# Performance work log

Measured on AMD Instinct MI355X. Metric: run time of the kernel, lower is better.

## Reference

```python
import jax, jax.numpy as jnp
import numpy as np
from jax import lax

B, C_IN, N, C_OUT, K = 16, 128, 2048, 256, 20
EPS = 1e-5


def setup_inputs() -> dict:
    key = jax.random.key(0)
    k1, k2 = jax.random.split(key)
    x = jax.random.normal(k1, (B, C_IN, N), dtype=jnp.float32)
    W = jax.random.normal(k2, (C_OUT, 2 * C_IN), dtype=jnp.float32) * (1.0 / np.sqrt(2 * C_IN))
    gamma = jnp.ones((C_OUT,), dtype=jnp.float32)
    beta = jnp.zeros((C_OUT,), dtype=jnp.float32)
    return {"x": x, "W": W, "gamma": gamma, "beta": beta, "k": K}


def _knn_inds(x, k):
    # squared pairwise distance: (B, N, N); computed with no grad (stop_gradient)
    xs = lax.stop_gradient(x)
    inner = jnp.einsum('bcn,bcm->bnm', xs, xs)
    sq = jnp.sum(xs * xs, axis=1)  # (B, N)
    pd = sq[:, :, None] - 2.0 * inner + sq[:, None, :]
    _, inds = lax.top_k(-pd, k)  # smallest distances -> (B, N, k)
    return inds


def reference(x, W, gamma, beta, k):
    knn = _knn_inds(x, k)                                   # (B, N, k) int
    # gather neighbours: neigh[b,c,n,j] = x[b,c,knn[b,n,j]]
    neigh = jax.vmap(lambda xb, kb: xb[:, kb])(x, knn)      # (B, C, N, k)
    central = jnp.broadcast_to(x[:, :, :, None], neigh.shape)
    edge = jnp.concatenate([central, neigh - central], axis=1)  # (B, 2C, N, k)
    # 1x1 conv (bias-free) as GEMM
    y = jnp.einsum('oc,bcnk->bonk', W, edge)                # (B, C_out, N, k)
    # BatchNorm2d (training-mode batch stats) + affine
    mean = jnp.mean(y, axis=(0, 2, 3), keepdims=True)
    var = jnp.var(y, axis=(0, 2, 3), keepdims=True)
    y = (y - mean) * lax.rsqrt(var + EPS)
    y = y * gamma[None, :, None, None] + beta[None, :, None, None]
    y = jax.nn.relu(y)
    return jnp.max(y, axis=3)                               # (B, C_out, N)
```

## Files before the change

kernel.cpp:

```cpp
#include <hip/hip_runtime.h>

#define B_   16
#define CIN  128
#define NPT  2048
#define COUT 256
#define KNN  20
#define KEEP 16
#define CAND 64
#define SIFT 32
#define EPS  1e-5f
#define DBIAS 256.0f

#define SQ_OFF   0ull
#define IDX_OFF  131072ull
#define UT_OFF   2752512ull
#define VT_OFF   36306944ull
#define GS_OFF   69861376ull
#define ST_OFF   69865472ull
#define AMAX_OFF 69871616ull
#define AMIN_OFF 103426048ull
#define WS_NEED_FUSED 136980480ull
#define XT_OFF   UT_OFF
#define XHT_OFF  VT_OFF

typedef _Float16 f16x8 __attribute__((ext_vector_type(8)));
typedef float    f32x4 __attribute__((ext_vector_type(4)));
typedef float    f32x2 __attribute__((ext_vector_type(2)));

__global__ __launch_bounds__(256) void prep_kernel(const float* __restrict__ x,
                                                   float* __restrict__ xT,
                                                   _Float16* __restrict__ xhT,
                                                   float* __restrict__ sqh) {
    __shared__ float Ls[128 * 68];
    __shared__ float ps[4 * 64];
    const int b = blockIdx.y, n0 = blockIdx.x * 64, t = threadIdx.x;
    const float* xb = x + (size_t)b * CIN * NPT;
    #pragma unroll
    for (int e = 0; e < 8; ++e) {
        int f = e * 256 + t;
        int c = f >> 4, n4 = (f & 15) << 2;
        *(float4*)&Ls[c * 68 + n4] = *(const float4*)&xb[(size_t)c * NPT + n0 + n4];
    }
    __syncthreads();
    {
        int nl = t & 63, part = t >> 6;
        float acc = 0.f;
        #pragma unroll
        for (int j = 0; j < 32; ++j) {
            float vh = (float)(_Float16)Ls[(part * 32 + j) * 68 + nl];
            acc += vh * vh;
        }
        ps[part * 64 + nl] = acc;
    }
    #pragma unroll
    for (int e = 0; e < 2; ++e) {
        int u = e * 256 + t;
        int nl = u >> 3, ck = (u & 7) << 4;
        float vv[16];
        #pragma unroll
        for (int j = 0; j < 16; ++j) vv[j] = Ls[(ck + j) * 68 + nl];
        size_t row = (size_t)b * NPT + n0 + nl;
        #pragma unroll
        for (int j = 0; j < 4; ++j) {
            float4 w = {vv[4 * j], vv[4 * j + 1], vv[4 * j + 2], vv[4 * j + 3]};
            *(float4*)&xT[row * CIN + ck + 4 * j] = w;
        }
        f16x8 h0, h1;
        #pragma unroll
        for (int j = 0; j < 8; ++j) { h0[j] = (_Float16)vv[j]; h1[j] = (_Float16)vv[8 + j]; }
        *(f16x8*)&xhT[row * CIN + ck] = h0;
        *(f16x8*)&xhT[row * CIN + ck + 8] = h1;
    }
    __syncthreads();
    if (t < 64) sqh[b * NPT + n0 + t] = ps[t] + ps[64 + t] + ps[128 + t] + ps[192 + t];
}

__global__ void wconv_kernel(const float* __restrict__ W,
                             _Float16* __restrict__ Wu,
                             _Float16* __restrict__ Wv) {
    int gid = blockIdx.x * 256 + threadIdx.x;
    int o = gid >> 7, c = gid & 127;
    float w1 = W[o * 256 + c], w2 = W[o * 256 + 128 + c];
    Wu[gid] = (_Float16)(w1 - w2);
    Wv[gid] = (_Float16)w2;
}

__device__ __forceinline__ void stage_pts(const _Float16* __restrict__ xhb,
                                          _Float16* buf, int base_n, int t) {
    const int l15 = t & 15, ks = t >> 6;
    const int quad = (t >> 4) & 3;
    const int c = ks * 32 + quad * 8;
    #pragma unroll
    for (int e = 0; e < 4; ++e) {
        const int n = base_n + e * 16 + l15;
        const _Float16* src = xhb + (size_t)n * CIN + c;
        _Float16* dst = buf + (size_t)(e * 256 + (t & 192)) * 8;
        __builtin_amdgcn_global_load_lds(
            (const __attribute__((address_space(1))) void*)src,
            (__attribute__((address_space(3))) void*)dst, 16, 0, 0);
    }
}

__device__ __forceinline__ void stage_tile16(const _Float16* __restrict__ srcl,
                                             _Float16* dsthalf) {
    #pragma unroll
    for (int e = 0; e < 4; ++e) {
        __builtin_amdgcn_global_load_lds(
            (const __attribute__((address_space(1))) void*)(srcl + e * 32),
            (__attribute__((address_space(3))) void*)(dsthalf + (size_t)e * 512),
            16, 0, 0);
    }
}

__global__ __launch_bounds__(256, 2) void knn_kernel(const _Float16* __restrict__ xhT,
                                                     const float* __restrict__ sqh,
                                                     int* __restrict__ surv_out) {
    __shared__ char smraw[59392];
    _Float16* bufA = (_Float16*)smraw;
    float*    sqm  = (float*)(smraw + 18432);

    const int id  = blockIdx.x;
    const int xcd = id & 7, qq = id >> 3;
    const int b   = xcd + ((qq >> 5) << 3);
    const int q0  = (qq & 31) * 64;
    const int t  = threadIdx.x;
    const int lane = t & 63, wv = t >> 6;
    const int l15 = lane & 15, quad = lane >> 4;
    const _Float16* xhb = xhT + (size_t)b * NPT * CIN;

    #pragma unroll
    for (int e = 0; e < 8; ++e)
        sqm[e * 256 + t] = sqh[b * NPT + e * 256 + t] + DBIAS;

    stage_pts(xhb, bufA, q0, t);
    __syncthreads();

    f16x8 af[4][4];
    #pragma unroll
    for (int qh = 0; qh < 4; ++qh)
        #pragma unroll
        for (int ks = 0; ks < 4; ++ks)
            af[qh][ks] = *(const f16x8*)(bufA + (size_t)((qh * 4 + ks) * 64 + lane) * 8);
    __syncthreads();

    _Float16* wbuf = (_Float16*)(smraw + 26624 + wv * 8192);
    float*    DtW  = (float*)(smraw + wv * 4608);
    const _Float16* srcl = xhb + (size_t)(wv * 16 + l15) * CIN + quad * 8;

    stage_tile16(srcl, wbuf);

    float bd[KEEP];
    #pragma unroll
    for (int i = 0; i < KEEP; ++i) bd[i] = 3.0e38f;

    #pragma unroll 1
    for (int ss = 0; ss < 32; ++ss) {
        const int mb = ss * 64 + wv * 16;
        asm volatile("s_waitcnt vmcnt(0)" ::: "memory");
        __builtin_amdgcn_sched_barrier(0);
        const _Float16* cur = wbuf + (ss & 1) * 2048;
        f16x8 bf[4];
        #pragma unroll
        for (int ks = 0; ks < 4; ++ks)
            bf[ks] = *(const f16x8*)(cur + ks * 512 + lane * 8);
        float sm_ = sqm[mb + l15];
        asm volatile("s_waitcnt lgkmcnt(0)" ::: "memory");
        __builtin_amdgcn_sched_barrier(0);
        if (ss < 31)
            stage_tile16(srcl + (size_t)(ss + 1) * 64 * CIN,
                         wbuf + ((ss + 1) & 1) * 2048);
        __builtin_amdgcn_sched_barrier(0);
        f32x4 acc[4];
        #pragma unroll
        for (int qh = 0; qh < 4; ++qh) acc[qh] = (f32x4){0.f, 0.f, 0.f, 0.f};
        #pragma unroll
        for (int ks = 0; ks < 4; ++ks)
            #pragma unroll
            for (int qh = 0; qh < 4; ++qh)
                acc[qh] = __builtin_amdgcn_mfma_f32_16x16x32_f16(af[qh][ks], bf[ks], acc[qh], 0, 0, 0);
        const unsigned om = (unsigned)(mb + l15);
        #pragma unroll
        for (int qh = 0; qh < 4; ++qh) {
            #pragma unroll
            for (int rg = 0; rg < 4; ++rg) {
                int q = qh * 16 + quad * 4 + rg;
                float d = sm_ - 2.f * acc[qh][rg];
                DtW[q * 18 + l15] = __uint_as_float((__float_as_uint(d) & 0xFFFFF800u) | om);
            }
        }
        float nk[16];
        {
            const float* myrow = DtW + lane * 18;
            #pragma unroll
            for (int p = 0; p < 8; ++p) {
                f32x2 v = *(const f32x2*)(myrow + 2 * p);
                nk[2 * p] = v[0]; nk[2 * p + 1] = v[1];
            }
        }
        #pragma unroll
        for (int kk = 2; kk <= 16; kk <<= 1) {
            #pragma unroll
            for (int j = kk >> 1; j > 0; j >>= 1) {
                #pragma unroll
                for (int i = 0; i < 16; ++i) {
                    int p = i ^ j;
                    if (p > i) {
                        float a = nk[i], c = nk[p];
                        float lo = fminf(a, c), hi = fmaxf(a, c);
                        if ((i & kk) == 0) { nk[i] = lo; nk[p] = hi; }
                        else               { nk[i] = hi; nk[p] = lo; }
                    }
                }
            }
        }
        #pragma unroll
        for (int i = 0; i < 16; ++i) bd[i] = fminf(bd[i], nk[15 - i]);
        #pragma unroll
        for (int j = 8; j > 0; j >>= 1) {
            #pragma unroll
            for (int i = 0; i < 16; ++i) {
                int p = i ^ j;
                if (p > i) {
                    float a = bd[i], c = bd[p];
                    bd[i] = fminf(a, c);
                    bd[p] = fmaxf(a, c);
                }
            }
        }
    }

    __syncthreads();

    float* Keys = (float*)smraw;
    #pragma unroll
    for (int i = 0; i < KEEP; ++i)
        Keys[lane * 65 + wv * KEEP + i] = bd[i];
    __syncthreads();
    {
        int cnt[KEEP];
        #pragma unroll
        for (int i = 0; i < KEEP; ++i) cnt[i] = 0;
        #pragma unroll 4
        for (int j = 0; j < CAND; ++j) {
            float kj = Keys[lane * 65 + j];
            #pragma unroll
            for (int i = 0; i < KEEP; ++i)
                cnt[i] += (kj < bd[i]) ? 1 : 0;
        }
        int* dst = surv_out + ((size_t)b * NPT + q0 + lane) * SIFT;
        #pragma unroll
        for (int i = 0; i < KEEP; ++i)
            if (cnt[i] < SIFT)
                dst[cnt[i]] = (int)(__float_as_uint(bd[i]) & 0x7FFu);
    }
}

__global__ __launch_bounds__(256, 4) void refine_kernel(const float* __restrict__ xT,
                                                        const int* __restrict__ surv,
                                                        int* __restrict__ knn_out) {
    __shared__ float  Qs[16 * 128];
    __shared__ int    sidx[16 * 32];
    __shared__ double ddL[16 * 32];
    const int id  = blockIdx.x;
    const int xcd = id & 7, qq = id >> 3;
    const int b   = xcd + ((qq >> 7) << 3);
    const int q0  = (qq & 127) * 16;
    const int t = threadIdx.x;
    const float* xTb = xT + (size_t)b * NPT * CIN;
    #pragma unroll
    for (int e = 0; e < 2; ++e)
        sidx[e * 256 + t] = surv[((size_t)b * NPT + q0) * SIFT + e * 256 + t];
    #pragma unroll
    for (int e = 0; e < 2; ++e) {
        int f = e * 256 + t;
        int row = f >> 5, c4 = (f & 31) << 2;
        *(float4*)&Qs[row * 128 + c4] = *(const float4*)&xTb[(size_t)(q0 + row) * CIN + c4];
    }
    __syncthreads();
    const int g = t >> 3, j = t & 7;
    #pragma unroll 1
    for (int it = 0; it < 16; ++it) {
        int pair = it * 32 + g;
        int q = pair >> 5, k = pair & 31;
        int m = sidx[q * 32 + k];
        const float* mrow = xTb + (size_t)m * CIN + j * 16;
        const float* qrow = Qs + q * 128 + j * 16;
        float4 a0 = *(const float4*)&mrow[0];
        float4 a1 = *(const float4*)&mrow[4];
        float4 a2 = *(const float4*)&mrow[8];
        float4 a3 = *(const float4*)&mrow[12];
        float4 c0 = *(const float4*)&qrow[0];
        float4 c1 = *(const float4*)&qrow[4];
        float4 c2 = *(const float4*)&qrow[8];
        float4 c3 = *(const float4*)&qrow[12];
        double ss = 0.0, d0;
        d0 = (double)c0.x - (double)a0.x; ss = fma(d0, d0, ss);
        d0 = (double)c0.y - (double)a0.y; ss = fma(d0, d0, ss);
        d0 = (double)c0.z - (double)a0.z; ss = fma(d0, d0, ss);
        d0 = (double)c0.w - (double)a0.w; ss = fma(d0, d0, ss);
        d0 = (double)c1.x - (double)a1.x; ss = fma(d0, d0, ss);
        d0 = (double)c1.y - (double)a1.y; ss = fma(d0, d0, ss);
        d0 = (double)c1.z - (double)a1.z; ss = fma(d0, d0, ss);
        d0 = (double)c1.w - (double)a1.w; ss = fma(d0, d0, ss);
        d0 = (double)c2.x - (double)a2.x; ss = fma(d0, d0, ss);
        d0 = (double)c2.y - (double)a2.y; ss = fma(d0, d0, ss);
        d0 = (double)c2.z - (double)a2.z; ss = fma(d0, d0, ss);
        d0 = (double)c2.w - (double)a2.w; ss = fma(d0, d0, ss);
        d0 = (double)c3.x - (double)a3.x; ss = fma(d0, d0, ss);
        d0 = (double)c3.y - (double)a3.y; ss = fma(d0, d0, ss);
        d0 = (double)c3.z - (double)a3.z; ss = fma(d0, d0, ss);
        d0 = (double)c3.w - (double)a3.w; ss = fma(d0, d0, ss);
        ss += __shfl_xor(ss, 1, 8);
        ss += __shfl_xor(ss, 2, 8);
        ss += __shfl_xor(ss, 4, 8);
        if (j == 0) ddL[q * 32 + k] = ss;
    }
    __syncthreads();
    const int q = t >> 4, kk = (t & 15) << 1;
    int* dst = knn_out + ((size_t)b * NPT + q0 + q) * KNN;
    #pragma unroll
    for (int e = 0; e < 2; ++e) {
        int k = kk + e;
        double mine = ddL[q * 32 + k];
        int c = 0;
        #pragma unroll 4
        for (int jx = 0; jx < SIFT; ++jx)
            c += (ddL[q * 32 + jx] < mine) ? 1 : 0;
        if (c < KNN) dst[c] = sidx[q * 32 + k];
    }
}

__global__ __launch_bounds__(256, 2) void knn_kernel_fb(const _Float16* __restrict__ xhT,
                                                        const float* __restrict__ xT,
                                                        const float* __restrict__ sqh,
                                                        int* __restrict__ knn_out) {
    __shared__ char smraw[59392];
    _Float16* bufA = (_Float16*)smraw;
    float*    sqm  = (float*)(smraw + 18432);

    const int b  = blockIdx.y;
    const int q0 = blockIdx.x * 64;
    const int t  = threadIdx.x;
    const int lane = t & 63, wv = t >> 6;
    const int l15 = lane & 15, quad = lane >> 4;
    const _Float16* xhb = xhT + (size_t)b * NPT * CIN;

    #pragma unroll
    for (int e = 0; e < 8; ++e)
        sqm[e * 256 + t] = sqh[b * NPT + e * 256 + t] + DBIAS;

    stage_pts(xhb, bufA, q0, t);
    __syncthreads();

    f16x8 af[4][4];
    #pragma unroll
    for (int qh = 0; qh < 4; ++qh)
        #pragma unroll
        for (int ks = 0; ks < 4; ++ks)
            af[qh][ks] = *(const f16x8*)(bufA + (size_t)((qh * 4 + ks) * 64 + lane) * 8);
    __syncthreads();

    _Float16* wbuf = (_Float16*)(smraw + 26624 + wv * 8192);
    float*    DtW  = (float*)(smraw + wv * 4608);
    const _Float16* srcl = xhb + (size_t)(wv * 16 + l15) * CIN + quad * 8;
    stage_tile16(srcl, wbuf);

    float bd[KEEP];
    #pragma unroll
    for (int i = 0; i < KEEP; ++i) bd[i] = 3.0e38f;

    #pragma unroll 1
    for (int ss = 0; ss < 32; ++ss) {
        const int mb = ss * 64 + wv * 16;
        asm volatile("s_waitcnt vmcnt(0)" ::: "memory");
        __builtin_amdgcn_sched_barrier(0);
        const _Float16* cur = wbuf + (ss & 1) * 2048;
        f16x8 bf[4];
        #pragma unroll
        for (int ks = 0; ks < 4; ++ks)
            bf[ks] = *(const f16x8*)(cur + ks * 512 + lane * 8);
        float sm_ = sqm[mb + l15];
        asm volatile("s_waitcnt lgkmcnt(0)" ::: "memory");
        __builtin_amdgcn_sched_barrier(0);
        if (ss < 31)
            stage_tile16(srcl + (size_t)(ss + 1) * 64 * CIN,
                         wbuf + ((ss + 1) & 1) * 2048);
        __builtin_amdgcn_sched_barrier(0);
        f32x4 acc[4];
        #pragma unroll
        for (int qh = 0; qh < 4; ++qh) acc[qh] = (f32x4){0.f, 0.f, 0.f, 0.f};
        #pragma unroll
        for (int ks = 0; ks < 4; ++ks)
            #pragma unroll
            for (int qh = 0; qh < 4; ++qh)
                acc[qh] = __builtin_amdgcn_mfma_f32_16x16x32_f16(af[qh][ks], bf[ks], acc[qh], 0, 0, 0);
        const unsigned om = (unsigned)(mb + l15);
        #pragma unroll
        for (int qh = 0; qh < 4; ++qh) {
            #pragma unroll
            for (int rg = 0; rg < 4; ++rg) {
                int q = qh * 16 + quad * 4 + rg;
                float d = sm_ - 2.f * acc[qh][rg];
                DtW[q * 18 + l15] = __uint_as_float((__float_as_uint(d) & 0xFFFFF800u) | om);
            }
        }
        float nk[16];
        {
            const float* myrow = DtW + lane * 18;
            #pragma unroll
            for (int p = 0; p < 8; ++p) {
                f32x2 v = *(const f32x2*)(myrow + 2 * p);
                nk[2 * p] = v[0]; nk[2 * p + 1] = v[1];
            }
        }
        #pragma unroll
        for (int kk = 2; kk <= 16; kk <<= 1) {
            #pragma unroll
            for (int j = kk >> 1; j > 0; j >>= 1) {
                #pragma unroll
                for (int i = 0; i < 16; ++i) {
                    int p = i ^ j;
                    if (p > i) {
                        float a = nk[i], c = nk[p];
                        float lo = fminf(a, c), hi = fmaxf(a, c);
                        if ((i & kk) == 0) { nk[i] = lo; nk[p] = hi; }
                        else               { nk[i] = hi; nk[p] = lo; }
                    }
                }
            }
        }
        #pragma unroll
        for (int i = 0; i < 16; ++i) bd[i] = fminf(bd[i], nk[15 - i]);
        #pragma unroll
        for (int j = 8; j > 0; j >>= 1) {
            #pragma unroll
            for (int i = 0; i < 16; ++i) {
                int p = i ^ j;
                if (p > i) {
                    float a = bd[i], c = bd[p];
                    bd[i] = fminf(a, c);
                    bd[p] = fmaxf(a, c);
                }
            }
        }
    }

    __syncthreads();

    float*  Keys = (float*)smraw;
    int*    Surv = (int*)(smraw + 16640);
    double* ddL  = (double*)(smraw + 25088);
    #pragma unroll
    for (int i = 0; i < KEEP; ++i)
        Keys[lane * 65 + wv * KEEP + i] = bd[i];
    __syncthreads();
    {
        int cnt[KEEP];
        #pragma unroll
        for (int i = 0; i < KEEP; ++i) cnt[i] = 0;
        #pragma unroll 4
        for (int j = 0; j < CAND; ++j) {
            float kj = Keys[lane * 65 + j];
            #pragma unroll
            for (int i = 0; i < KEEP; ++i)
                cnt[i] += (kj < bd[i]) ? 1 : 0;
        }
        __syncthreads();
        #pragma unroll
        for (int i = 0; i < KEEP; ++i)
            if (cnt[i] < SIFT)
                Surv[lane * 33 + cnt[i]] = (int)(__float_as_uint(bd[i]) & 0x7FFu);
    }
    __syncthreads();

    int ms[8];
    #pragma unroll
    for (int k = 0; k < 8; ++k) ms[k] = Surv[lane * 33 + wv * 8 + k] & 2047;
    double dd8[8];
    #pragma unroll
    for (int k = 0; k < 8; ++k) dd8[k] = 0.0;
    const float* xTb = xT + (size_t)b * NPT * CIN;
    const float* qrow = xTb + (size_t)(q0 + lane) * CIN;
    #pragma unroll 1
    for (int ch = 0; ch < 8; ++ch) {
        double qd[16];
        #pragma unroll
        for (int j = 0; j < 4; ++j) {
            float4 qv = *(const float4*)&qrow[ch * 16 + 4 * j];
            qd[4 * j] = (double)qv.x; qd[4 * j + 1] = (double)qv.y;
            qd[4 * j + 2] = (double)qv.z; qd[4 * j + 3] = (double)qv.w;
        }
        #pragma unroll
        for (int k = 0; k < 8; ++k) {
            const float* mrow = xTb + (size_t)ms[k] * CIN + ch * 16;
            float4 ma = *(const float4*)&mrow[0];
            float4 mb2 = *(const float4*)&mrow[4];
            float4 mc = *(const float4*)&mrow[8];
            float4 md = *(const float4*)&mrow[12];
            double ss = dd8[k], d0;
            d0 = qd[0]  - (double)ma.x;  ss = fma(d0, d0, ss);
            d0 = qd[1]  - (double)ma.y;  ss = fma(d0, d0, ss);
            d0 = qd[2]  - (double)ma.z;  ss = fma(d0, d0, ss);
            d0 = qd[3]  - (double)ma.w;  ss = fma(d0, d0, ss);
            d0 = qd[4]  - (double)mb2.x; ss = fma(d0, d0, ss);
            d0 = qd[5]  - (double)mb2.y; ss = fma(d0, d0, ss);
            d0 = qd[6]  - (double)mb2.z; ss = fma(d0, d0, ss);
            d0 = qd[7]  - (double)mb2.w; ss = fma(d0, d0, ss);
            d0 = qd[8]  - (double)mc.x;  ss = fma(d0, d0, ss);
            d0 = qd[9]  - (double)mc.y;  ss = fma(d0, d0, ss);
            d0 = qd[10] - (double)mc.z;  ss = fma(d0, d0, ss);
            d0 = qd[11] - (double)mc.w;  ss = fma(d0, d0, ss);
            d0 = qd[12] - (double)md.x;  ss = fma(d0, d0, ss);
            d0 = qd[13] - (double)md.y;  ss = fma(d0, d0, ss);
            d0 = qd[14] - (double)md.z;  ss = fma(d0, d0, ss);
            d0 = qd[15] - (double)md.w;  ss = fma(d0, d0, ss);
            dd8[k] = ss;
        }
    }
    #pragma unroll
    for (int k = 0; k < 8; ++k) ddL[lane * 33 + wv * 8 + k] = dd8[k];
    __syncthreads();
    int* dst = knn_out + ((size_t)b * NPT + q0 + lane) * KNN;
    #pragma unroll
    for (int k = 0; k < 8; ++k) {
        int c = 0;
        #pragma unroll 4
        for (int j = 0; j < SIFT; ++j)
            c += (ddL[lane * 33 + j] < dd8[k]) ? 1 : 0;
        if (c < KNN) dst[c] = ms[k];
    }
}

__global__ __launch_bounds__(256) void uv_gemm_h(const _Float16* __restrict__ xhT,
                                                 const _Float16* __restrict__ Wu,
                                                 const _Float16* __restrict__ Wv,
                                                 float* __restrict__ uT,
                                                 float* __restrict__ vT) {
    __shared__ _Float16 Bx[8192];
    const int b = blockIdx.y, n0 = blockIdx.x * 64, t = threadIdx.x;
    const int lane = t & 63, w = t >> 6, l15 = lane & 15, quad = lane >> 4;
    stage_pts(xhT + (size_t)b * NPT * CIN, Bx, n0, t);
    __syncthreads();
    f16x8 bf[4];
    #pragma unroll
    for (int ks = 0; ks < 4; ++ks)
        bf[ks] = *(const f16x8*)(Bx + (size_t)((w * 4 + ks) * 64 + lane) * 8);
    const int n = n0 + w * 16 + l15;
    #pragma unroll 1
    for (int ot = 0; ot < 16; ++ot) {
        const _Float16* wu = Wu + (size_t)(ot * 16 + l15) * 128 + quad * 8;
        const _Float16* wv2 = Wv + (size_t)(ot * 16 + l15) * 128 + quad * 8;
        f32x4 au = (f32x4){0.f, 0.f, 0.f, 0.f};
        f32x4 av = (f32x4){0.f, 0.f, 0.f, 0.f};
        #pragma unroll
        for (int ks = 0; ks < 4; ++ks) {
            f16x8 a_u = *(const f16x8*)(wu + ks * 32);
            f16x8 a_v = *(const f16x8*)(wv2 + ks * 32);
            au = __builtin_amdgcn_mfma_f32_16x16x32_f16(a_u, bf[ks], au, 0, 0, 0);
            av = __builtin_amdgcn_mfma_f32_16x16x32_f16(a_v, bf[ks], av, 0, 0, 0);
        }
        size_t base = ((size_t)b * NPT + n) * COUT + ot * 16 + quad * 4;
        *(f32x4*)&uT[base] = au;
        *(f32x4*)&vT[base] = av;
    }
}

__global__ __launch_bounds__(256) void uv_gemm(const float* __restrict__ x,
                                               const float* __restrict__ W,
                                               float* __restrict__ uT,
                                               float* __restrict__ vT) {
    __shared__ float Ax[32 * 64];
    __shared__ float Bu[32 * 68];
    __shared__ float Bv[32 * 68];
    const int b  = blockIdx.z;
    const int n0 = blockIdx.x * 64;
    const int o0 = blockIdx.y * 64;
    const int t  = threadIdx.x;
    const int tx = t & 15, ty = t >> 4;
    const float* xb = x + (size_t)b * CIN * NPT;
    float au[4][4], av_[4][4];
    #pragma unroll
    for (int i = 0; i < 4; ++i)
        #pragma unroll
        for (int j = 0; j < 4; ++j) { au[i][j] = 0.f; av_[i][j] = 0.f; }
    #pragma unroll 1
    for (int kc = 0; kc < 4; ++kc) {
        const int c0 = kc * 32;
        __syncthreads();
        #pragma unroll
        for (int e = 0; e < 2; ++e) {
            int f = e * 256 + t;
            int cz = f >> 4, ni = (f & 15) << 2;
            *(float4*)&Ax[(cz << 6) + ni] = *(const float4*)&xb[(size_t)(c0 + cz) * NPT + n0 + ni];
        }
        #pragma unroll
        for (int e = 0; e < 8; ++e) {
            int ii = e * 256 + t;
            int cz = ii & 31, oj = ii >> 5;
            float w1 = W[(size_t)(o0 + oj) * 256 + c0 + cz];
            float w2 = W[(size_t)(o0 + oj) * 256 + 128 + c0 + cz];
            Bu[cz * 68 + oj] = w1 - w2;
            Bv[cz * 68 + oj] = w2;
        }
        __syncthreads();
        #pragma unroll 8
        for (int cz = 0; cz < 32; ++cz) {
            const float4 a4 = *(const float4*)&Ax[(cz << 6) + (tx << 2)];
            float bu0 = Bu[cz * 68 + (ty << 2) + 0], bv0 = Bv[cz * 68 + (ty << 2) + 0];
            float bu1 = Bu[cz * 68 + (ty << 2) + 1], bv1 = Bv[cz * 68 + (ty << 2) + 1];
            float bu2 = Bu[cz * 68 + (ty << 2) + 2], bv2 = Bv[cz * 68 + (ty << 2) + 2];
            float bu3 = Bu[cz * 68 + (ty << 2) + 3], bv3 = Bv[cz * 68 + (ty << 2) + 3];
            au[0][0] += a4.x * bu0; au[0][1] += a4.x * bu1; au[0][2] += a4.x * bu2; au[0][3] += a4.x * bu3;
            au[1][0] += a4.y * bu0; au[1][1] += a4.y * bu1; au[1][2] += a4.y * bu2; au[1][3] += a4.y * bu3;
            au[2][0] += a4.z * bu0; au[2][1] += a4.z * bu1; au[2][2] += a4.z * bu2; au[2][3] += a4.z * bu3;
            au[3][0] += a4.w * bu0; au[3][1] += a4.w * bu1; au[3][2] += a4.w * bu2; au[3][3] += a4.w * bu3;
            av_[0][0] += a4.x * bv0; av_[0][1] += a4.x * bv1; av_[0][2] += a4.x * bv2; av_[0][3] += a4.x * bv3;
            av_[1][0] += a4.y * bv0; av_[1][1] += a4.y * bv1; av_[1][2] += a4.y * bv2; av_[1][3] += a4.y * bv3;
            av_[2][0] += a4.z * bv0; av_[2][1] += a4.z * bv1; av_[2][2] += a4.z * bv2; av_[2][3] += a4.z * bv3;
            av_[3][0] += a4.w * bv0; av_[3][1] += a4.w * bv1; av_[3][2] += a4.w * bv2; av_[3][3] += a4.w * bv3;
        }
    }
    #pragma unroll
    for (int i = 0; i < 4; ++i) {
        int n = n0 + (tx << 2) + i;
        size_t base = ((size_t)b * NPT + n) * COUT + o0 + (ty << 2);
        float4 u4 = {au[i][0], au[i][1], au[i][2], au[i][3]};
        float4 v4 = {av_[i][0], av_[i][1], av_[i][2], av_[i][3]};
        *(float4*)&uT[base] = u4;
        *(float4*)&vT[base] = v4;
    }
}

__global__ __launch_bounds__(256) void gather_stats(const float* __restrict__ uT,
                                                    const float* __restrict__ vT,
                                                    const int* __restrict__ knn_in,
                                                    double* __restrict__ gsum,
                                                    float* __restrict__ aMax,
                                                    float* __restrict__ aMin) {
    __shared__ int sidx[16 * KNN];
    const int id  = blockIdx.x;
    const int xcd = id & 7, qq = id >> 3;
    const int b   = xcd + ((qq >> 7) << 3);
    const int inner = qq & 127;
    const int n0  = (inner >> 2) * 64 + (inner & 3) * 16;
    const int o   = threadIdx.x;
    for (int e = o; e < 16 * KNN; e += 256)
        sidx[e] = knn_in[((size_t)b * NPT + n0) * KNN + e];
    __syncthreads();
    const float* ub = uT + ((size_t)b * NPT + n0) * COUT + o;
    const float* vb = vT + (size_t)b * NPT * COUT + o;
    float* amx = aMax + ((size_t)b * NPT + n0) * COUT + o;
    float* amn = aMin + ((size_t)b * NPT + n0) * COUT + o;
    double s1 = 0.0, s2 = 0.0;
    #pragma unroll 1
    for (int s = 0; s < 16; ++s) {
        float u = ub[(size_t)s * COUT];
        float vmax = -3e38f, vmin = 3e38f, vsum = 0.f, vsq = 0.f;
        #pragma unroll
        for (int j = 0; j < KNN; ++j) {
            float v = vb[(size_t)sidx[s * KNN + j] * COUT];
            vmax = fmaxf(vmax, v);
            vmin = fminf(vmin, v);
            vsum += v;
            vsq = fmaf(v, v, vsq);
        }
        s1 += 20.0 * (double)u + (double)vsum;
        s2 += 20.0 * (double)u * (double)u + 2.0 * (double)u * (double)vsum + (double)vsq;
        float y1 = u + vmax;
        float y2 = u + vmin;
        __builtin_nontemporal_store(y1, &amx[(size_t)s * COUT]);
        __builtin_nontemporal_store(y2, &amn[(size_t)s * COUT]);
    }
    atomicAdd(&gsum[o], s1);
    atomicAdd(&gsum[COUT + o], s2);
}

__global__ __launch_bounds__(256) void stats_kernel(const float* __restrict__ uT,
                                                    const float* __restrict__ vT,
                                                    const int* __restrict__ knn_in,
                                                    double* __restrict__ gsum) {
    __shared__ int sidx[64 * KNN];
    const int b  = blockIdx.y;
    const int n0 = blockIdx.x * 64;
    const int o  = threadIdx.x;
    for (int e = o; e < 64 * KNN; e += 256)
        sidx[e] = knn_in[((size_t)b * NPT + n0) * KNN + e];
    __syncthreads();
    const float* ub = uT + ((size_t)b * NPT + n0) * COUT + o;
    const float* vb = vT + (size_t)b * NPT * COUT + o;
    double s1 = 0.0, s2 = 0.0;
    #pragma unroll 1
    for (int s = 0; s < 64; ++s) {
        float u = ub[(size_t)s * COUT];
        #pragma unroll
        for (int j = 0; j < KNN; ++j) {
            float y = u + vb[(size_t)sidx[s * KNN + j] * COUT];
            s1 += (double)y;
            s2 = fma((double)y, (double)y, s2);
        }
    }
    atomicAdd(&gsum[o], s1);
    atomicAdd(&gsum[COUT + o], s2);
}

__global__ void finalize_kernel(const double* __restrict__ gsum,
                                const float* __restrict__ gamma,
                                const float* __restrict__ beta,
                                float* __restrict__ st) {
    const int o = threadIdx.x;
    const double M = (double)B_ * NPT * KNN;
    double mean = gsum[o] / M;
    double var  = gsum[COUT + o] / M - mean * mean;
    float inv = 1.0f / sqrtf((float)var + EPS);
    float s = gamma[o] * inv;
    st[o] = s;
    st[COUT + o] = beta[o] - (float)mean * s;
}

__global__ __launch_bounds__(256, 2) void out2_kernel(const float* __restrict__ aMax,
                                                      const float* __restrict__ aMin,
                                                      const float* __restrict__ st,
                                                      float* __restrict__ out) {
    __shared__ float zt[256 * 68];
    const int b  = blockIdx.y;
    const int n0 = blockIdx.x * 64;
    const int o  = threadIdx.x;
    const float s  = st[o];
    const float tt = st[COUT + o];
    const float* amx = aMax + ((size_t)b * NPT + n0) * COUT + o;
    const float* amn = aMin + ((size_t)b * NPT + n0) * COUT + o;
    #pragma unroll 2
    for (int si = 0; si < 64; ++si) {
        float y1 = amx[(size_t)si * COUT];
        float y2 = amn[(size_t)si * COUT];
        float z1 = fmaxf(s * y1 + tt, 0.f);
        float z2 = fmaxf(s * y2 + tt, 0.f);
        zt[o * 68 + si] = fmaxf(z1, z2);
    }
    __syncthreads();
    float* dst = out + ((size_t)b * COUT + o) * NPT + n0;
    #pragma unroll
    for (int i = 0; i < 16; ++i)
        *(float4*)&dst[i * 4] = *(const float4*)&zt[o * 68 + i * 4];
}

__global__ __launch_bounds__(256, 2) void out_kernel(const float* __restrict__ uT,
                                                     const float* __restrict__ vT,
                                                     const int* __restrict__ knn_in,
                                                     const float* __restrict__ st,
                                                     float* __restrict__ out) {
    __shared__ int sidx[64 * KNN];
    __shared__ float zt[256 * 68];
    const int b  = blockIdx.y;
    const int n0 = blockIdx.x * 64;
    const int o  = threadIdx.x;
    for (int e = o; e < 64 * KNN; e += 256)
        sidx[e] = knn_in[((size_t)b * NPT + n0) * KNN + e];
    __syncthreads();
    const float s  = st[o];
    const float tt = st[COUT + o];
    const float* ub = uT + ((size_t)b * NPT + n0) * COUT + o;
    const float* vb = vT + (size_t)b * NPT * COUT + o;
    #pragma unroll 1
    for (int si = 0; si < 64; ++si) {
        float u = ub[(size_t)si * COUT];
        float ymax = -3e38f, ymin = 3e38f;
        #pragma unroll
        for (int j = 0; j < KNN; ++j) {
            float y = u + vb[(size_t)sidx[si * KNN + j] * COUT];
            ymax = fmaxf(ymax, y);
            ymin = fminf(ymin, y);
        }
        float z1 = fmaxf(s * ymax + tt, 0.f);
        float z2 = fmaxf(s * ymin + tt, 0.f);
        zt[o * 68 + si] = fmaxf(z1, z2);
    }
    __syncthreads();
    float* dst = out + ((size_t)b * COUT + o) * NPT + n0;
    #pragma unroll
    for (int i = 0; i < 16; ++i)
        *(float4*)&dst[i * 4] = *(const float4*)&zt[o * 68 + i * 4];
}

extern "C" void kernel_launch(void* const* d_in, const int* in_sizes, int n_in,
                              void* d_out, int out_size, void* d_ws, size_t ws_size,
                              hipStream_t stream) {
    const float* x     = (const float*)d_in[0];
    const float* W     = (const float*)d_in[1];
    const float* gamma = (const float*)d_in[2];
    const float* beta  = (const float*)d_in[3];
    float* out = (float*)d_out;
    char* ws = (char*)d_ws;
    float*     sqh  = (float*)(ws + SQ_OFF);
    int*       idx  = (int*)(ws + IDX_OFF);
    float*     uT   = (float*)(ws + UT_OFF);
    float*     vT   = (float*)(ws + VT_OFF);
    double*    gsum = (double*)(ws + GS_OFF);
    float*     st   = (float*)(ws + ST_OFF);
    float*     aMax = (float*)(ws + AMAX_OFF);
    float*     aMin = (float*)(ws + AMIN_OFF);
    const bool fused = (ws_size >= WS_NEED_FUSED);

    hipMemsetAsync(gsum, 0, 2 * COUT * sizeof(double), stream);
    if (fused) {
        float*    xT  = (float*)(ws + AMAX_OFF);
        _Float16* xhT = (_Float16*)(ws + AMAX_OFF + 16777216ull);
        _Float16* Wu  = (_Float16*)(ws + AMAX_OFF + 25165824ull);
        _Float16* Wv  = (_Float16*)(ws + AMAX_OFF + 25231360ull);
        int*      svG = (int*)(ws + UT_OFF);
        prep_kernel<<<dim3(32, 16), 256, 0, stream>>>(x, xT, xhT, sqh);
        wconv_kernel<<<128, 256, 0, stream>>>(W, Wu, Wv);
        knn_kernel<<<512, 256, 0, stream>>>(xhT, sqh, svG);
        refine_kernel<<<2048, 256, 0, stream>>>(xT, svG, idx);
        uv_gemm_h<<<dim3(32, 16), 256, 0, stream>>>(xhT, Wu, Wv, uT, vT);
        gather_stats<<<2048, 256, 0, stream>>>(uT, vT, idx, gsum, aMax, aMin);
        finalize_kernel<<<1, 256, 0, stream>>>(gsum, gamma, beta, st);
        out2_kernel<<<dim3(32, 16), 256, 0, stream>>>(aMax, aMin, st, out);
    } else {
        float*    xT  = (float*)(ws + XT_OFF);
        _Float16* xhT = (_Float16*)(ws + XHT_OFF);
        prep_kernel<<<dim3(32, 16), 256, 0, stream>>>(x, xT, xhT, sqh);
        knn_kernel_fb<<<dim3(32, 16), 256, 0, stream>>>(xhT, xT, sqh, idx);
        uv_gemm<<<dim3(32, 4, 16), 256, 0, stream>>>(x, W, uT, vT);
        stats_kernel<<<dim3(32, 16), 256, 0, stream>>>(uT, vT, idx, gsum);
        finalize_kernel<<<1, 256, 0, stream>>>(gsum, gamma, beta, st);
        out_kernel<<<dim3(32, 16), 256, 0, stream>>>(uT, vT, idx, st, out);
    }
}
```

Measured before the change: 307.6 us.

## Halve knn query tile to 32 points, doubling blocks and occupancy

The knn kernel now processes 32 query points per block instead of 64, which doubles the grid to 1024 blocks, shrinks shared memory and raises launch bounds to 4 blocks per CU. Each lane sorts 8 candidates per tile instead of 16, merged into the upper half of its top-16 list. The final sift now compares across 128 keys (8 sub-lists per query) instead of 64. The double-buffered prefetch of the next tile is removed in favour of a synchronous load each iteration, relying on higher occupancy to hide latency; it also re-reads the candidate points twice as often across blocks.

```diff
diff --git a/kernel.cpp b/kernel.cpp
--- a/kernel.cpp
+++ b/kernel.cpp
@@ -6,7 +6,6 @@
 #define COUT 256
 #define KNN  20
 #define KEEP 16
-#define CAND 64
 #define SIFT 32
 #define EPS  1e-5f
 #define DBIAS 256.0f
@@ -101,6 +100,22 @@
     }
 }
 
+__device__ __forceinline__ void stage_pts32(const _Float16* __restrict__ xhb,
+                                            _Float16* buf, int base_n, int t) {
+    const int l15 = t & 15, ks = t >> 6;
+    const int quad = (t >> 4) & 3;
+    const int c = ks * 32 + quad * 8;
+    #pragma unroll
+    for (int e = 0; e < 2; ++e) {
+        const int n = base_n + e * 16 + l15;
+        const _Float16* src = xhb + (size_t)n * CIN + c;
+        _Float16* dst = buf + (size_t)(e * 256 + (t & 192)) * 8;
+        __builtin_amdgcn_global_load_lds(
+            (const __attribute__((address_space(1))) void*)src,
+            (__attribute__((address_space(3))) void*)dst, 16, 0, 0);
+    }
+}
+
 __device__ __forceinline__ void stage_tile16(const _Float16* __restrict__ srcl,
                                              _Float16* dsthalf) {
     #pragma unroll
@@ -112,18 +127,18 @@
     }
 }
 
-__global__ __launch_bounds__(256, 2) void knn_kernel(const _Float16* __restrict__ xhT,
+__global__ __launch_bounds__(256, 4) void knn_kernel(const _Float16* __restrict__ xhT,
                                                      const float* __restrict__ sqh,
                                                      int* __restrict__ surv_out) {
-    __shared__ char smraw[59392];
+    __shared__ char smraw[33792];
     _Float16* bufA = (_Float16*)smraw;
-    float*    sqm  = (float*)(smraw + 18432);
+    float*    sqm  = (float*)(smraw + 25600);
 
     const int id  = blockIdx.x;
     const int xcd = id & 7, qq = id >> 3;
-    const int b   = xcd + ((qq >> 5) << 3);
-    const int q0  = (qq & 31) * 64;
-    const int t  = threadIdx.x;
+    const int b   = xcd + ((qq >> 6) << 3);
+    const int q0  = (qq & 63) * 32;
+    const int t   = threadIdx.x;
     const int lane = t & 63, wv = t >> 6;
     const int l15 = lane & 15, quad = lane >> 4;
     const _Float16* xhb = xhT + (size_t)b * NPT * CIN;
@@ -132,22 +147,20 @@
     for (int e = 0; e < 8; ++e)
         sqm[e * 256 + t] = sqh[b * NPT + e * 256 + t] + DBIAS;
 
-    stage_pts(xhb, bufA, q0, t);
-    __syncthreads();
-
-    f16x8 af[4][4];
-    #pragma unroll
-    for (int qh = 0; qh < 4; ++qh)
-        #pragma unroll
-        for (int ks = 0; ks < 4; ++ks)
-            af[qh][ks] = *(const f16x8*)(bufA + (size_t)((qh * 4 + ks) * 64 + lane) * 8);
-    __syncthreads();
-
-    _Float16* wbuf = (_Float16*)(smraw + 26624 + wv * 8192);
-    float*    DtW  = (float*)(smraw + wv * 4608);
+    stage_pts32(xhb, bufA, q0, t);
+    __syncthreads();
+
+    f16x8 af0[4], af1[4];
+    #pragma unroll
+    for (int ks = 0; ks < 4; ++ks) {
+        af0[ks] = *(const f16x8*)(bufA + (size_t)((ks)*64 + lane) * 8);
+        af1[ks] = *(const f16x8*)(bufA + (size_t)((4 + ks) * 64 + lane) * 8);
+    }
+    __syncthreads();
+
+    _Float16* wbuf = (_Float16*)(smraw + 9216 + wv * 4096);
+    float*    DtW  = (float*)(smraw + wv * 2304);
     const _Float16* srcl = xhb + (size_t)(wv * 16 + l15) * CIN + quad * 8;
-
-    stage_tile16(srcl, wbuf);
 
     float bd[KEEP];
     #pragma unroll
@@ -156,53 +169,49 @@
     #pragma unroll 1
     for (int ss = 0; ss < 32; ++ss) {
         const int mb = ss * 64 + wv * 16;
+        stage_tile16(srcl + (size_t)ss * 64 * CIN, wbuf);
+        float sm_ = sqm[mb + l15];
         asm volatile("s_waitcnt vmcnt(0)" ::: "memory");
         __builtin_amdgcn_sched_barrier(0);
-        const _Float16* cur = wbuf + (ss & 1) * 2048;
-        f16x8 bf[4];
-        #pragma unroll
-        for (int ks = 0; ks < 4; ++ks)
-            bf[ks] = *(const f16x8*)(cur + ks * 512 + lane * 8);
-        float sm_ = sqm[mb + l15];
-        asm volatile("s_waitcnt lgkmcnt(0)" ::: "memory");
-        __builtin_amdgcn_sched_barrier(0);
-        if (ss < 31)
-            stage_tile16(srcl + (size_t)(ss + 1) * 64 * CIN,
-                         wbuf + ((ss + 1) & 1) * 2048);
-        __builtin_amdgcn_sched_barrier(0);
-        f32x4 acc[4];
-        #pragma unroll
-        for (int qh = 0; qh < 4; ++qh) acc[qh] = (f32x4){0.f, 0.f, 0.f, 0.f};
-        #pragma unroll
-        for (int ks = 0; ks < 4; ++ks)
-            #pragma unroll
-            for (int qh = 0; qh < 4; ++qh)
-                acc[qh] = __builtin_amdgcn_mfma_f32_16x16x32_f16(af[qh][ks], bf[ks], acc[qh], 0, 0, 0);
+        f16x8 bf0 = *(const f16x8*)(wbuf + 0 * 512 + lane * 8);
+        f16x8 bf1 = *(const f16x8*)(wbuf + 1 * 512 + lane * 8);
+        f16x8 bf2 = *(const f16x8*)(wbuf + 2 * 512 + lane * 8);
+        f16x8 bf3 = *(const f16x8*)(wbuf + 3 * 512 + lane * 8);
+        f32x4 acc0 = (f32x4){0.f, 0.f, 0.f, 0.f};
+        f32x4 acc1 = (f32x4){0.f, 0.f, 0.f, 0.f};
+        acc0 = __builtin_amdgcn_mfma_f32_16x16x32_f16(af0[0], bf0, acc0, 0, 0, 0);
+        acc1 = __builtin_amdgcn_mfma_f32_16x16x32_f16(af1[0], bf0, acc1, 0, 0, 0);
+        acc0 = __builtin_amdgcn_mfma_f32_16x16x32_f16(af0[1], bf1, acc0, 0, 0, 0);
+        acc1 = __builtin_amdgcn_mfma_f32_16x16x32_f16(af1[1], bf1, acc1, 0, 0, 0);
+        acc0 = __builtin_amdgcn_mfma_f32_16x16x32_f16(af0[2], bf2, acc0, 0, 0, 0);
+        acc1 = __builtin_amdgcn_mfma_f32_16x16x32_f16(af1[2], bf2, acc1, 0, 0, 0);
+        acc0 = __builtin_amdgcn_mfma_f32_16x16x32_f16(af0[3], bf3, acc0, 0, 0, 0);
+        acc1 = __builtin_amdgcn_mfma_f32_16x16x32_f16(af1[3], bf3, acc1, 0, 0, 0);
         const unsigned om = (unsigned)(mb + l15);
         #pragma unroll
-        for (int qh = 0; qh < 4; ++qh) {
-            #pragma unroll
-            for (int rg = 0; rg < 4; ++rg) {
-                int q = qh * 16 + quad * 4 + rg;
-                float d = sm_ - 2.f * acc[qh][rg];
-                DtW[q * 18 + l15] = __uint_as_float((__float_as_uint(d) & 0xFFFFF800u) | om);
-            }
-        }
-        float nk[16];
+        for (int rg = 0; rg < 4; ++rg) {
+            float d0 = sm_ - 2.f * acc0[rg];
+            DtW[(quad * 4 + rg) * 18 + l15] =
+                __uint_as_float((__float_as_uint(d0) & 0xFFFFF800u) | om);
+            float d1 = sm_ - 2.f * acc1[rg];
+            DtW[(16 + quad * 4 + rg) * 18 + l15] =
+                __uint_as_float((__float_as_uint(d1) & 0xFFFFF800u) | om);
+        }
+        float nk[8];
         {
-            const float* myrow = DtW + lane * 18;
-            #pragma unroll
-            for (int p = 0; p < 8; ++p) {
+            const float* myrow = DtW + (lane & 31) * 18 + (lane >> 5) * 8;
+            #pragma unroll
+            for (int p = 0; p < 4; ++p) {
                 f32x2 v = *(const f32x2*)(myrow + 2 * p);
                 nk[2 * p] = v[0]; nk[2 * p + 1] = v[1];
             }
         }
         #pragma unroll
-        for (int kk = 2; kk <= 16; kk <<= 1) {
+        for (int kk = 2; kk <= 8; kk <<= 1) {
             #pragma unroll
             for (int j = kk >> 1; j > 0; j >>= 1) {
                 #pragma unroll
-                for (int i = 0; i < 16; ++i) {
+                for (int i = 0; i < 8; ++i) {
                     int p = i ^ j;
                     if (p > i) {
                         float a = nk[i], c = nk[p];
@@ -214,7 +223,7 @@
             }
         }
         #pragma unroll
-        for (int i = 0; i < 16; ++i) bd[i] = fminf(bd[i], nk[15 - i]);
+        for (int i = 0; i < 8; ++i) bd[8 + i] = fminf(bd[8 + i], nk[7 - i]);
         #pragma unroll
         for (int j = 8; j > 0; j >>= 1) {
             #pragma unroll
@@ -232,22 +241,24 @@
     __syncthreads();
 
     float* Keys = (float*)smraw;
+    const int qy  = lane & 31;
+    const int sub = wv * 2 + (lane >> 5);
     #pragma unroll
     for (int i = 0; i < KEEP; ++i)
-        Keys[lane * 65 + wv * KEEP + i] = bd[i];
+        Keys[qy * 129 + sub * KEEP + i] = bd[i];
     __syncthreads();
     {
         int cnt[KEEP];
         #pragma unroll
         for (int i = 0; i < KEEP; ++i) cnt[i] = 0;
         #pragma unroll 4
-        for (int j = 0; j < CAND; ++j) {
-            float kj = Keys[lane * 65 + j];
+        for (int j = 0; j < 128; ++j) {
+            float kj = Keys[qy * 129 + j];
             #pragma unroll
             for (int i = 0; i < KEEP; ++i)
                 cnt[i] += (kj < bd[i]) ? 1 : 0;
         }
-        int* dst = surv_out + ((size_t)b * NPT + q0 + lane) * SIFT;
+        int* dst = surv_out + ((size_t)b * NPT + q0 + qy) * SIFT;
         #pragma unroll
         for (int i = 0; i < KEEP; ++i)
             if (cnt[i] < SIFT)
@@ -459,7 +470,7 @@
         #pragma unroll
         for (int i = 0; i < KEEP; ++i) cnt[i] = 0;
         #pragma unroll 4
-        for (int j = 0; j < CAND; ++j) {
+        for (int j = 0; j < 64; ++j) {
             float kj = Keys[lane * 65 + j];
             #pragma unroll
             for (int i = 0; i < KEEP; ++i)
@@ -810,7 +821,7 @@
         int*      svG = (int*)(ws + UT_OFF);
         prep_kernel<<<dim3(32, 16), 256, 0, stream>>>(x, xT, xhT, sqh);
         wconv_kernel<<<128, 256, 0, stream>>>(W, Wu, Wv);
-        knn_kernel<<<512, 256, 0, stream>>>(xhT, sqh, svG);
+        knn_kernel<<<1024, 256, 0, stream>>>(xhT, sqh, svG);
         refine_kernel<<<2048, 256, 0, stream>>>(xT, svG, idx);
         uv_gemm_h<<<dim3(32, 16), 256, 0, stream>>>(xhT, Wu, Wv, uT, vT);
         gather_stats<<<2048, 256, 0, stream>>>(uT, vT, idx, gsum, aMax, aMin);
```

Measured after the change: 364.5 us. 1.19x slower.

## Split KNN candidate scan across eight waves per block, drop double buffering

Applied to the files above, without the earlier changes.

The KNN kernel now runs 512 threads per block, so eight waves share the candidate columns and the outer loop takes 16 steps instead of 32. Each wave loads its tile synchronously into a single LDS buffer instead of prefetching the next tile into a double buffer. The final per-query merge therefore ranks 128 kept candidates instead of 64. This trades the load/compute overlap, and possibly registers under the tighter launch bound, for more waves to hide latency. The LDS footprint also grows.

```diff
diff --git a/kernel.cpp b/kernel.cpp
--- a/kernel.cpp
+++ b/kernel.cpp
@@ -6,7 +6,6 @@
 #define COUT 256
 #define KNN  20
 #define KEEP 16
-#define CAND 64
 #define SIFT 32
 #define EPS  1e-5f
 #define DBIAS 256.0f
@@ -112,27 +111,27 @@
     }
 }
 
-__global__ __launch_bounds__(256, 2) void knn_kernel(const _Float16* __restrict__ xhT,
+__global__ __launch_bounds__(512, 4) void knn_kernel(const _Float16* __restrict__ xhT,
                                                      const float* __restrict__ sqh,
                                                      int* __restrict__ surv_out) {
-    __shared__ char smraw[59392];
+    __shared__ char smraw[77824];
     _Float16* bufA = (_Float16*)smraw;
-    float*    sqm  = (float*)(smraw + 18432);
+    float*    sqm  = (float*)(smraw + 69632);
 
     const int id  = blockIdx.x;
     const int xcd = id & 7, qq = id >> 3;
     const int b   = xcd + ((qq >> 5) << 3);
     const int q0  = (qq & 31) * 64;
-    const int t  = threadIdx.x;
+    const int t   = threadIdx.x;
     const int lane = t & 63, wv = t >> 6;
     const int l15 = lane & 15, quad = lane >> 4;
     const _Float16* xhb = xhT + (size_t)b * NPT * CIN;
 
     #pragma unroll
-    for (int e = 0; e < 8; ++e)
-        sqm[e * 256 + t] = sqh[b * NPT + e * 256 + t] + DBIAS;
-
-    stage_pts(xhb, bufA, q0, t);
+    for (int e = 0; e < 4; ++e)
+        sqm[e * 512 + t] = sqh[b * NPT + e * 512 + t] + DBIAS;
+
+    if (wv < 4) stage_pts(xhb, bufA, q0, t);
     __syncthreads();
 
     f16x8 af[4][4];
@@ -143,41 +142,35 @@
             af[qh][ks] = *(const f16x8*)(bufA + (size_t)((qh * 4 + ks) * 64 + lane) * 8);
     __syncthreads();
 
-    _Float16* wbuf = (_Float16*)(smraw + 26624 + wv * 8192);
+    _Float16* wbuf = (_Float16*)(smraw + 36864 + wv * 4096);
     float*    DtW  = (float*)(smraw + wv * 4608);
     const _Float16* srcl = xhb + (size_t)(wv * 16 + l15) * CIN + quad * 8;
 
-    stage_tile16(srcl, wbuf);
-
     float bd[KEEP];
     #pragma unroll
     for (int i = 0; i < KEEP; ++i) bd[i] = 3.0e38f;
 
     #pragma unroll 1
-    for (int ss = 0; ss < 32; ++ss) {
-        const int mb = ss * 64 + wv * 16;
+    for (int ss = 0; ss < 16; ++ss) {
+        const int mb = ss * 128 + wv * 16;
+        stage_tile16(srcl + (size_t)ss * 128 * CIN, wbuf);
+        float sm_ = sqm[mb + l15];
         asm volatile("s_waitcnt vmcnt(0)" ::: "memory");
         __builtin_amdgcn_sched_barrier(0);
-        const _Float16* cur = wbuf + (ss & 1) * 2048;
-        f16x8 bf[4];
-        #pragma unroll
-        for (int ks = 0; ks < 4; ++ks)
-            bf[ks] = *(const f16x8*)(cur + ks * 512 + lane * 8);
-        float sm_ = sqm[mb + l15];
-        asm volatile("s_waitcnt lgkmcnt(0)" ::: "memory");
-        __builtin_amdgcn_sched_barrier(0);
-        if (ss < 31)
-            stage_tile16(srcl + (size_t)(ss + 1) * 64 * CIN,
-                         wbuf + ((ss + 1) & 1) * 2048);
-        __builtin_amdgcn_sched_barrier(0);
+        f16x8 bf0 = *(const f16x8*)(wbuf + 0 * 512 + lane * 8);
+        f16x8 bf1 = *(const f16x8*)(wbuf + 1 * 512 + lane * 8);
+        f16x8 bf2 = *(const f16x8*)(wbuf + 2 * 512 + lane * 8);
+        f16x8 bf3 = *(const f16x8*)(wbuf + 3 * 512 + lane * 8);
         f32x4 acc[4];
         #pragma unroll
         for (int qh = 0; qh < 4; ++qh) acc[qh] = (f32x4){0.f, 0.f, 0.f, 0.f};
         #pragma unroll
-        for (int ks = 0; ks < 4; ++ks)
-            #pragma unroll
-            for (int qh = 0; qh < 4; ++qh)
-                acc[qh] = __builtin_amdgcn_mfma_f32_16x16x32_f16(af[qh][ks], bf[ks], acc[qh], 0, 0, 0);
+        for (int qh = 0; qh < 4; ++qh) {
+            acc[qh] = __builtin_amdgcn_mfma_f32_16x16x32_f16(af[qh][0], bf0, acc[qh], 0, 0, 0);
+            acc[qh] = __builtin_amdgcn_mfma_f32_16x16x32_f16(af[qh][1], bf1, acc[qh], 0, 0, 0);
+            acc[qh] = __builtin_amdgcn_mfma_f32_16x16x32_f16(af[qh][2], bf2, acc[qh], 0, 0, 0);
+            acc[qh] = __builtin_amdgcn_mfma_f32_16x16x32_f16(af[qh][3], bf3, acc[qh], 0, 0, 0);
+        }
         const unsigned om = (unsigned)(mb + l15);
         #pragma unroll
         for (int qh = 0; qh < 4; ++qh) {
@@ -234,15 +227,15 @@
     float* Keys = (float*)smraw;
     #pragma unroll
     for (int i = 0; i < KEEP; ++i)
-        Keys[lane * 65 + wv * KEEP + i] = bd[i];
+        Keys[lane * 129 + wv * KEEP + i] = bd[i];
     __syncthreads();
     {
         int cnt[KEEP];
         #pragma unroll
         for (int i = 0; i < KEEP; ++i) cnt[i] = 0;
         #pragma unroll 4
-        for (int j = 0; j < CAND; ++j) {
-            float kj = Keys[lane * 65 + j];
+        for (int j = 0; j < 128; ++j) {
+            float kj = Keys[lane * 129 + j];
             #pragma unroll
             for (int i = 0; i < KEEP; ++i)
                 cnt[i] += (kj < bd[i]) ? 1 : 0;
@@ -459,7 +452,7 @@
         #pragma unroll
         for (int i = 0; i < KEEP; ++i) cnt[i] = 0;
         #pragma unroll 4
-        for (int j = 0; j < CAND; ++j) {
+        for (int j = 0; j < 64; ++j) {
             float kj = Keys[lane * 65 + j];
             #pragma unroll
             for (int i = 0; i < KEEP; ++i)
@@ -810,7 +803,7 @@
         int*      svG = (int*)(ws + UT_OFF);
         prep_kernel<<<dim3(32, 16), 256, 0, stream>>>(x, xT, xhT, sqh);
         wconv_kernel<<<128, 256, 0, stream>>>(W, Wu, Wv);
-        knn_kernel<<<512, 256, 0, stream>>>(xhT, sqh, svG);
+        knn_kernel<<<512, 512, 0, stream>>>(xhT, sqh, svG);
         refine_kernel<<<2048, 256, 0, stream>>>(xT, svG, idx);
         uv_gemm_h<<<dim3(32, 16), 256, 0, stream>>>(xhT, Wu, Wv, uT, vT);
         gather_stats<<<2048, 256, 0, stream>>>(uT, vT, idx, gsum, aMax, aMin);
```

New measurement: 343.3 us. +11.6%, slower.
